# Kernel optimization log

Measured on AMD Instinct MI355X. Metric: run time of the kernel, lower is better.

## Reference

```python
import jax, jax.numpy as jnp
import numpy as np

ALPHA = 10.0
K = 10
BN_EPS = 1e-5


def _conv3d(x, w, b, pad):
    # x: [N,C,D,H,W], w: [O,I,kd,kh,kw]
    y = jax.lax.conv_general_dilated(
        x, w, window_strides=(1, 1, 1),
        padding=[(pad, pad)] * 3,
        dimension_numbers=('NCDHW', 'OIDHW', 'NCDHW'))
    return y + b[None, :, None, None, None]


def _bn(x, gamma, beta, mean, var):
    c = (None, slice(None), None, None, None)
    return gamma[c] * (x - mean[c]) * jax.lax.rsqrt(var[c] + BN_EPS) + beta[c]


def setup_inputs() -> dict:
    key = jax.random.key(0)
    ks = jax.random.split(key, 12)
    B, D, H, W = 1, 32, 32, 32
    LAT = 8
    M = 4096  # stored database vectors
    inp = {
        'bg_prob': jax.random.uniform(ks[0], (B, 1, D, H, W), jnp.float32),
        'ed_prob': jax.random.uniform(ks[1], (B, 1, D, H, W), jnp.float32),
        'context_mask': jnp.ones((B, D, H, W), dtype=bool),
        # conv1: 2 -> 16, k3
        'w1': jax.random.normal(ks[2], (16, 2, 3, 3, 3), jnp.float32) * 0.1,
        'b1': jnp.zeros((16,), jnp.float32),
        'g1': jnp.ones((16,), jnp.float32),
        'be1': jnp.zeros((16,), jnp.float32),
        'm1': jnp.zeros((16,), jnp.float32),
        'v1': jnp.ones((16,), jnp.float32),
        # conv2: 16 -> 32, k3
        'w2': jax.random.normal(ks[3], (32, 16, 3, 3, 3), jnp.float32) * 0.05,
        'b2': jnp.zeros((32,), jnp.float32),
        'g2': jnp.ones((32,), jnp.float32),
        'be2': jnp.zeros((32,), jnp.float32),
        'm2': jnp.zeros((32,), jnp.float32),
        'v2': jnp.ones((32,), jnp.float32),
        # conv3: 32 -> latent_dim, k1
        'w3': jax.random.normal(ks[4], (LAT, 32, 1, 1, 1), jnp.float32) * 0.1,
        'b3': jnp.zeros((LAT,), jnp.float32),
    }
    db = jax.random.normal(ks[5], (M, LAT), jnp.float32)
    db = db / jnp.maximum(jnp.linalg.norm(db, axis=1, keepdims=True), 1e-12)
    inp['db_feats'] = db
    inp['db_labels'] = jax.random.uniform(ks[6], (M,), jnp.float32)
    return inp


def reference(bg_prob, ed_prob, context_mask,
              w1, b1, g1, be1, m1, v1,
              w2, b2, g2, be2, m2, v2,
              w3, b3, db_feats, db_labels):
    # --- query encoder (BatchNorm in inference mode) ---
    x = jnp.concatenate([bg_prob, ed_prob], axis=1)              # [B,2,D,H,W]
    x = jax.nn.relu(_bn(_conv3d(x, w1, b1, 1), g1, be1, m1, v1))
    x = jax.nn.relu(_bn(_conv3d(x, w2, b2, 1), g2, be2, m2, v2))
    lat = _conv3d(x, w3, b3, 0)                                   # [B,C,D,H,W]
    # F.normalize(dim=1), eps=1e-12
    lat = lat / jnp.maximum(jnp.linalg.norm(lat, axis=1, keepdims=True), 1e-12)
    B, C, D, H, W = lat.shape
    q = lat.transpose(0, 2, 3, 4, 1).reshape(-1, C)               # [N,C]
    # --- exact L2 kNN (FAISS IndexFlatL2 returns squared distances) ---
    d2 = (jnp.sum(q * q, axis=1, keepdims=True)
          + jnp.sum(db_feats * db_feats, axis=1)[None, :]
          - 2.0 * q @ db_feats.T)                                 # [N,M]
    neg_top, idx = jax.lax.top_k(-d2, K)                          # k smallest
    dists = -neg_top                                              # [N,K]
    w = jnp.exp(-ALPHA * dists)
    lbl = db_labels[idx]                                          # [N,K] gather
    pred = jnp.sum(w * lbl, axis=1) / (jnp.sum(w, axis=1) + 1e-8)
    # NOTE: original view(B,2,D,H,W) is inconsistent (N=B*D*H*W preds);
    # return the consistent [B,D,H,W].
    return pred.reshape(B, D, H, W)
```

## Files before the change

kernel.cpp:

```cpp
#include <hip/hip_runtime.h>

#define ALPHA 10.0f
#define BN_EPS 1e-5f
#define NVOX 32768
#define MDB 4096
#define CAP 128

typedef __attribute__((ext_vector_type(8))) short short8;
typedef __attribute__((ext_vector_type(16))) float f32x16;

__device__ __forceinline__ unsigned short bfr(float x) {
  unsigned u = __float_as_uint(x);
  return (unsigned short)((u + 0x7FFFu + ((u >> 16) & 1u)) >> 16);
}
__device__ __forceinline__ void split3(float x, unsigned short& h,
                                       unsigned short& m, unsigned short& l) {
  h = bfr(x);
  float fh = __uint_as_float((unsigned)h << 16);
  float x1 = x - fh;
  m = bfr(x1);
  float fm = __uint_as_float((unsigned)m << 16);
  l = bfr(x1 - fm);
}

__device__ __forceinline__ f32x16 d2_tile(short8 a1, short8 a2, short8 a3,
                                          short8 a4, short8 b1, short8 b3,
                                          short8 b4) {
  f32x16 acc = {};
  acc = __builtin_amdgcn_mfma_f32_32x32x16_bf16(a4, b4, acc, 0, 0, 0);
  acc = __builtin_amdgcn_mfma_f32_32x32x16_bf16(a3, b3, acc, 0, 0, 0);
  acc = __builtin_amdgcn_mfma_f32_32x32x16_bf16(a2, b1, acc, 0, 0, 0);
  acc = __builtin_amdgcn_mfma_f32_32x32x16_bf16(a1, b1, acc, 0, 0, 0);
  return acc;
}

__device__ __forceinline__ float fmin3(float a, float b, float c) {
  return fminf(fminf(a, b), c);
}

#define INSERT2(d, va, vb)                                              \
  do {                                                                  \
    float _lo = fminf((va), (vb)), _hi = fmaxf((va), (vb));             \
    _Pragma("unroll")                                                   \
    for (int _k = 9; _k >= 2; --_k)                                     \
      d[_k] = fmin3(d[_k], fmaxf(d[_k - 1], _lo), fmaxf(d[_k - 2], _hi)); \
    d[1] = fmin3(d[1], fmaxf(d[0], _lo), _hi);                          \
    d[0] = fminf(d[0], _lo);                                            \
  } while (0)

__global__ __launch_bounds__(128) void k_conv1p(
    const float* __restrict__ bg, const float* __restrict__ ed,
    const float* __restrict__ w1, const float* __restrict__ b1,
    const float* __restrict__ g1, const float* __restrict__ be1,
    const float* __restrict__ m1, const float* __restrict__ v1,
    float* __restrict__ A, const float* __restrict__ db,
    unsigned short* __restrict__ DBH, unsigned short* __restrict__ DBM,
    unsigned short* __restrict__ DBL, unsigned short* __restrict__ DB4) {
  int t = threadIdx.x;
  if (blockIdx.x >= 256) {
    int j = (blockIdx.x - 256) * 128 + t;
    float4 x0 = ((const float4*)(db + (size_t)j * 8))[0];
    float4 x1 = ((const float4*)(db + (size_t)j * 8))[1];
    float x[8] = {x0.x, x0.y, x0.z, x0.w, x1.x, x1.y, x1.z, x1.w};
    float ss = x[0] * x[0];
#pragma unroll
    for (int i = 1; i < 8; ++i) ss = fmaf(x[i], x[i], ss);
    short8 sh = {}, sm = {}, sl = {};
#pragma unroll
    for (int i = 0; i < 8; ++i) {
      unsigned short h, m, l;
      split3(-2.f * x[i], h, m, l);
      sh[i] = (short)h; sm[i] = (short)m; sl[i] = (short)l;
    }
    unsigned short dh, dm, dl;
    split3(ss, dh, dm, dl);
    short8 s4 = {};
    s4[0] = (short)dh; s4[1] = (short)dm; s4[2] = (short)dl;
    s4[3] = (short)0x3F80; s4[4] = (short)0x3F80; s4[5] = (short)0x3F80;
    *(short8*)(DBH + (size_t)j * 8) = sh;
    *(short8*)(DBM + (size_t)j * 8) = sm;
    *(short8*)(DBL + (size_t)j * 8) = sl;
    *(short8*)(DB4 + (size_t)j * 8) = s4;
    return;
  }
  __shared__ float wT[54 * 16];
  __shared__ float sc[16], shs[16];
  for (int i = t; i < 864; i += 128) {
    int o = i & 15, r = i >> 4;
    wT[i] = w1[o * 54 + r];
  }
  if (t < 16) {
    float s = g1[t] * rsqrtf(v1[t] + BN_EPS);
    sc[t] = s;
    shs[t] = (b1[t] - m1[t]) * s + be1[t];
  }
  __syncthreads();
  int v = blockIdx.x * 128 + t;
  int x = v & 31, y = (v >> 5) & 31, z = v >> 10;
  float acc[16];
#pragma unroll
  for (int o = 0; o < 16; ++o) acc[o] = 0.f;
#pragma unroll 1
  for (int k = 0; k < 27; ++k) {
    int dz = k / 9 - 1, dy = (k / 3) % 3 - 1, dx = k % 3 - 1;
    int zz = z + dz, yy = y + dy, xx = x + dx;
    bool inb = (unsigned)zz < 32u && (unsigned)yy < 32u && (unsigned)xx < 32u;
    int vv = zz * 1024 + yy * 32 + xx;
#pragma unroll
    for (int c = 0; c < 2; ++c) {
      const float* in = c ? ed : bg;
      float val = inb ? in[vv] : 0.f;
      const float4* wp = (const float4*)&wT[(c * 27 + k) * 16];
      float4 wa = wp[0], wb = wp[1], wc = wp[2], wd = wp[3];
      acc[0] = fmaf(val, wa.x, acc[0]);  acc[1] = fmaf(val, wa.y, acc[1]);
      acc[2] = fmaf(val, wa.z, acc[2]);  acc[3] = fmaf(val, wa.w, acc[3]);
      acc[4] = fmaf(val, wb.x, acc[4]);  acc[5] = fmaf(val, wb.y, acc[5]);
      acc[6] = fmaf(val, wb.z, acc[6]);  acc[7] = fmaf(val, wb.w, acc[7]);
      acc[8] = fmaf(val, wc.x, acc[8]);  acc[9] = fmaf(val, wc.y, acc[9]);
      acc[10] = fmaf(val, wc.z, acc[10]); acc[11] = fmaf(val, wc.w, acc[11]);
      acc[12] = fmaf(val, wd.x, acc[12]); acc[13] = fmaf(val, wd.y, acc[13]);
      acc[14] = fmaf(val, wd.z, acc[14]); acc[15] = fmaf(val, wd.w, acc[15]);
    }
  }
#pragma unroll
  for (int o = 0; o < 16; ++o) {
    float y2 = fmaf(acc[o], sc[o], shs[o]);
    A[o * NVOX + v] = y2 > 0.f ? y2 : 0.f;
  }
}

__global__ __launch_bounds__(256) void k_conv2(
    const float* __restrict__ A, const float* __restrict__ w2,
    const float* __restrict__ b2, const float* __restrict__ g2,
    const float* __restrict__ be2, const float* __restrict__ m2,
    const float* __restrict__ v2, float* __restrict__ B) {
  __shared__ float wT[432 * 8];
  __shared__ float sc[8], shs[8];
  int t = threadIdx.x;
  int og = blockIdx.x >> 7;
  int vb = blockIdx.x & 127;
  for (int i = t; i < 3456; i += 256) {
    int o = i & 7, r = i >> 3;
    wT[i] = w2[(og * 8 + o) * 432 + r];
  }
  if (t < 8) {
    int o = og * 8 + t;
    float s = g2[o] * rsqrtf(v2[o] + BN_EPS);
    sc[t] = s;
    shs[t] = (b2[o] - m2[o]) * s + be2[o];
  }
  __syncthreads();
  int v = vb * 256 + t;
  int x = v & 31, y = (v >> 5) & 31, z = v >> 10;
  float acc[8];
#pragma unroll
  for (int o = 0; o < 8; ++o) acc[o] = 0.f;
#pragma unroll 1
  for (int k = 0; k < 27; ++k) {
    int dz = k / 9 - 1, dy = (k / 3) % 3 - 1, dx = k % 3 - 1;
    int zz = z + dz, yy = y + dy, xx = x + dx;
    bool inb = (unsigned)zz < 32u && (unsigned)yy < 32u && (unsigned)xx < 32u;
    int vv = zz * 1024 + yy * 32 + xx;
#pragma unroll
    for (int ci = 0; ci < 16; ++ci) {
      float val = inb ? A[ci * NVOX + vv] : 0.f;
      const float4* wp = (const float4*)&wT[(ci * 27 + k) * 8];
      float4 wa = wp[0], wb = wp[1];
      acc[0] = fmaf(val, wa.x, acc[0]); acc[1] = fmaf(val, wa.y, acc[1]);
      acc[2] = fmaf(val, wa.z, acc[2]); acc[3] = fmaf(val, wa.w, acc[3]);
      acc[4] = fmaf(val, wb.x, acc[4]); acc[5] = fmaf(val, wb.y, acc[5]);
      acc[6] = fmaf(val, wb.z, acc[6]); acc[7] = fmaf(val, wb.w, acc[7]);
    }
  }
#pragma unroll
  for (int o = 0; o < 8; ++o) {
    float y2 = fmaf(acc[o], sc[o], shs[o]);
    B[(og * 8 + o) * NVOX + v] = y2 > 0.f ? y2 : 0.f;
  }
}

__global__ __launch_bounds__(128) void k_conv3q(
    const float* __restrict__ B, const float* __restrict__ w3,
    const float* __restrict__ b3, unsigned short* __restrict__ QH,
    unsigned short* __restrict__ QM, unsigned short* __restrict__ QL,
    unsigned short* __restrict__ Q4) {
  __shared__ float wT[32 * 8];
  __shared__ float bL[8];
  int t = threadIdx.x;
  for (int i = t; i < 256; i += 128) {
    int o = i & 7, ci = i >> 3;
    wT[i] = w3[o * 32 + ci];
  }
  if (t < 8) bL[t] = b3[t];
  __syncthreads();
  int v = blockIdx.x * 128 + t;
  float lat[8];
#pragma unroll
  for (int o = 0; o < 8; ++o) lat[o] = bL[o];
#pragma unroll 4
  for (int ci = 0; ci < 32; ++ci) {
    float val = B[ci * NVOX + v];
    const float4* wp = (const float4*)&wT[ci * 8];
    float4 wa = wp[0], wb = wp[1];
    lat[0] = fmaf(val, wa.x, lat[0]); lat[1] = fmaf(val, wa.y, lat[1]);
    lat[2] = fmaf(val, wa.z, lat[2]); lat[3] = fmaf(val, wa.w, lat[3]);
    lat[4] = fmaf(val, wb.x, lat[4]); lat[5] = fmaf(val, wb.y, lat[5]);
    lat[6] = fmaf(val, wb.z, lat[6]); lat[7] = fmaf(val, wb.w, lat[7]);
  }
  float n2 = 0.f;
#pragma unroll
  for (int o = 0; o < 8; ++o) n2 = fmaf(lat[o], lat[o], n2);
  float inv = 1.f / fmaxf(sqrtf(n2), 1e-12f);
  float q[8];
#pragma unroll
  for (int o = 0; o < 8; ++o) q[o] = lat[o] * inv;
  float qq = q[0] * q[0];
#pragma unroll
  for (int o = 1; o < 8; ++o) qq = fmaf(q[o], q[o], qq);
  short8 sh = {}, sm = {}, sl = {};
#pragma unroll
  for (int o = 0; o < 8; ++o) {
    unsigned short h, m, l;
    split3(q[o], h, m, l);
    sh[o] = (short)h; sm[o] = (short)m; sl[o] = (short)l;
  }
  unsigned short qh, qm, ql;
  split3(qq, qh, qm, ql);
  short8 s4 = {};
  s4[0] = (short)0x3F80; s4[1] = (short)0x3F80; s4[2] = (short)0x3F80;
  s4[3] = (short)qh; s4[4] = (short)qm; s4[5] = (short)ql;
  *(short8*)(QH + (size_t)v * 8) = sh;
  *(short8*)(QM + (size_t)v * 8) = sm;
  *(short8*)(QL + (size_t)v * 8) = sl;
  *(short8*)(Q4 + (size_t)v * 8) = s4;
}

__global__ __launch_bounds__(512) void k_knn_fused(
    const unsigned short* __restrict__ QH, const unsigned short* __restrict__ QM,
    const unsigned short* __restrict__ QL, const unsigned short* __restrict__ Q4,
    const unsigned short* __restrict__ DBH, const unsigned short* __restrict__ DBM,
    const unsigned short* __restrict__ DBL, const unsigned short* __restrict__ DB4,
    const float* __restrict__ labels, float* __restrict__ out) {
  __shared__ float smem[2 * 32 * (CAP + 1)];
  __shared__ float T0L[32];
  __shared__ int cnt[32];
  float (*listd)[CAP + 1] = (float (*)[CAP + 1])smem;
  int (*listi)[CAP + 1] = (int (*)[CAP + 1])(smem + 32 * (CAP + 1));
  float (*lds_top)[10][32] = (float (*)[10][32])smem;
  int t = threadIdx.x, w = t >> 6, l = t & 63;
  int lo32 = l & 31, hi = l >> 5;
  int q = blockIdx.x * 32 + lo32;
  if (t < 32) cnt[t] = 0;
  short8 zz = {};
  short8 b1 = *(const short8*)((hi ? QM : QH) + (size_t)q * 8);
  short8 b3 = *(const short8*)((hi ? QL : QH) + (size_t)q * 8);
  short8 b4v = *(const short8*)(Q4 + (size_t)q * 8);
  short8 b4 = hi ? zz : b4v;
  int r0 = w * 512;

  float d[10];
#pragma unroll
  for (int k = 0; k < 10; ++k) d[k] = 3.4e38f;
#pragma unroll 1
  for (int tt = 0; tt < 4; ++tt) {
    int r = r0 + tt * 32 + lo32;
    short8 a1 = *(const short8*)(DBH + (size_t)r * 8);
    short8 a2 = *(const short8*)(DBM + (size_t)r * 8);
    short8 a3 = *(const short8*)((hi ? DBH : DBL) + (size_t)r * 8);
    short8 a4 = *(const short8*)(DB4 + (size_t)r * 8);
    f32x16 acc = d2_tile(a1, a2, a3, a4, b1, b3, b4);
#pragma unroll
    for (int p = 0; p < 8; ++p) INSERT2(d, acc[2 * p], acc[2 * p + 1]);
  }
  {
    float e[10];
#pragma unroll
    for (int k = 0; k < 10; ++k) e[k] = __shfl_xor(d[k], 32);
#pragma unroll
    for (int k = 0; k < 10; k += 2) INSERT2(d, e[k], e[k + 1]);
  }
  if (l < 32) {
#pragma unroll
    for (int k = 0; k < 10; ++k) lds_top[w][k][lo32] = d[k];
  }
  __syncthreads();
  if (t < 32) {
    float m[10];
#pragma unroll
    for (int k = 0; k < 10; ++k) m[k] = 3.4e38f;
#pragma unroll 1
    for (int w2 = 0; w2 < 8; ++w2) {
#pragma unroll
      for (int k2 = 0; k2 < 10; k2 += 2)
        INSERT2(m, lds_top[w2][k2][t], lds_top[w2][k2 + 1][t]);
    }
    T0L[t] = m[9];
  }
  __syncthreads();
  float T0q = T0L[lo32];

#pragma unroll 1
  for (int tt = 0; tt < 16; ++tt) {
    int r = r0 + tt * 32 + lo32;
    short8 a1 = *(const short8*)(DBH + (size_t)r * 8);
    short8 a2 = *(const short8*)(DBM + (size_t)r * 8);
    short8 a3 = *(const short8*)((hi ? DBH : DBL) + (size_t)r * 8);
    short8 a4 = *(const short8*)(DB4 + (size_t)r * 8);
    f32x16 acc = d2_tile(a1, a2, a3, a4, b1, b3, b4);
    int rb = r0 + tt * 32 + 4 * hi;
#pragma unroll
    for (int i = 0; i < 16; ++i) {
      float d2v = acc[i];
      bool p = d2v <= T0q;
      if (__any(p)) {
        if (p) {
          int slot = atomicAdd(&cnt[lo32], 1);
          if (slot < CAP) {
            listd[lo32][slot] = d2v;
            listi[lo32][slot] = rb + (i & 3) + 8 * (i >> 2);
          }
        }
      }
    }
  }
  __syncthreads();

  {
    int qc = t >> 4, s0 = t & 15;
    int n = min(cnt[qc], CAP);
    for (int s = s0; s < n; s += 16) {
      int idx = listi[qc][s];
      ((float*)listi[qc])[s] = labels[idx];
    }
  }
  __syncthreads();

  if (t < 32) {
    int n = min(cnt[t], CAP);
    float dd[10];
#pragma unroll
    for (int k = 0; k < 10; ++k) dd[k] = 3.4e38f;
    int j = 0;
#pragma unroll 1
    for (; j + 1 < n; j += 2) INSERT2(dd, listd[t][j], listd[t][j + 1]);
    if (j < n) INSERT2(dd, listd[t][j], 3.4e38f);
    float Tv = dd[9];
    const float C2 = -14.4269504088896340736f;
    float num = 0.f, den = 0.f;
#pragma unroll 1
    for (int j2 = 0; j2 < n; ++j2) {
      float v = listd[t][j2];
      if (v <= Tv) {
        float e = exp2f(v * C2);
        den += e;
        num = fmaf(e, ((float*)listi[t])[j2], num);
      }
    }
    out[blockIdx.x * 32 + t] = num / (den + 1e-8f);
  }
}

extern "C" void kernel_launch(void* const* d_in, const int* in_sizes, int n_in,
                              void* d_out, int out_size, void* d_ws, size_t ws_size,
                              hipStream_t stream) {
  const float* bg = (const float*)d_in[0];
  const float* ed = (const float*)d_in[1];
  const float* w1 = (const float*)d_in[3];
  const float* b1 = (const float*)d_in[4];
  const float* g1 = (const float*)d_in[5];
  const float* be1 = (const float*)d_in[6];
  const float* m1 = (const float*)d_in[7];
  const float* v1 = (const float*)d_in[8];
  const float* w2 = (const float*)d_in[9];
  const float* b2 = (const float*)d_in[10];
  const float* g2 = (const float*)d_in[11];
  const float* be2 = (const float*)d_in[12];
  const float* m2 = (const float*)d_in[13];
  const float* v2 = (const float*)d_in[14];
  const float* w3 = (const float*)d_in[15];
  const float* b3 = (const float*)d_in[16];
  const float* db = (const float*)d_in[17];
  const float* labels = (const float*)d_in[18];
  float* out = (float*)d_out;

  char* ws = (char*)d_ws;
  const size_t MB = 1024 * 1024;
  float* A = (float*)(ws + 0);
  float* B = (float*)(ws + 2 * MB);
  unsigned short* QH = (unsigned short*)(ws + 0);
  unsigned short* QM = QH + (size_t)NVOX * 8;
  unsigned short* QL = QM + (size_t)NVOX * 8;
  unsigned short* Q4 = QL + (size_t)NVOX * 8;
  unsigned short* DBH = (unsigned short*)(ws + 6 * MB);
  unsigned short* DBM = DBH + (size_t)MDB * 8;
  unsigned short* DBL = DBM + (size_t)MDB * 8;
  unsigned short* DB4 = DBL + (size_t)MDB * 8;

  k_conv1p<<<288, 128, 0, stream>>>(bg, ed, w1, b1, g1, be1, m1, v1, A, db,
                                    DBH, DBM, DBL, DB4);
  k_conv2<<<4 * 128, 256, 0, stream>>>(A, w2, b2, g2, be2, m2, v2, B);
  k_conv3q<<<256, 128, 0, stream>>>(B, w3, b3, QH, QM, QL, Q4);
  k_knn_fused<<<NVOX / 32, 512, 0, stream>>>(QH, QM, QL, Q4, DBH, DBM, DBL,
                                             DB4, labels, out);
}
```

Before: 115.7 us.

## Fuse 1x1 conv and query normalization into kNN kernel, parallelize label weighting

The separate conv3q kernel is removed. Each kNN block now computes the 1x1 conv, L2 normalization and bf16 three-way split for its 32 queries in shared memory, which saves a launch and the round trip of query data through global memory. The final weighted sum is split across 16 threads per query with a partial-sum reduction, instead of one thread doing a serial label gather. Conv1 moves to 256-thread blocks, and the warp-uniform __any check around candidate insertion is dropped. The cost is extra syncs and shared-memory work inside the kNN kernel, and smem aliasing that has to stay correct.

```diff
diff --git a/kernel.cpp b/kernel.cpp
--- a/kernel.cpp
+++ b/kernel.cpp
@@ -48,7 +48,7 @@
     d[0] = fminf(d[0], _lo);                                            \
   } while (0)
 
-__global__ __launch_bounds__(128) void k_conv1p(
+__global__ __launch_bounds__(256) void k_conv1p(
     const float* __restrict__ bg, const float* __restrict__ ed,
     const float* __restrict__ w1, const float* __restrict__ b1,
     const float* __restrict__ g1, const float* __restrict__ be1,
@@ -57,8 +57,8 @@
     unsigned short* __restrict__ DBH, unsigned short* __restrict__ DBM,
     unsigned short* __restrict__ DBL, unsigned short* __restrict__ DB4) {
   int t = threadIdx.x;
-  if (blockIdx.x >= 256) {
-    int j = (blockIdx.x - 256) * 128 + t;
+  if (blockIdx.x >= 128) {
+    int j = (blockIdx.x - 128) * 256 + t;
     float4 x0 = ((const float4*)(db + (size_t)j * 8))[0];
     float4 x1 = ((const float4*)(db + (size_t)j * 8))[1];
     float x[8] = {x0.x, x0.y, x0.z, x0.w, x1.x, x1.y, x1.z, x1.w};
@@ -85,7 +85,7 @@
   }
   __shared__ float wT[54 * 16];
   __shared__ float sc[16], shs[16];
-  for (int i = t; i < 864; i += 128) {
+  for (int i = t; i < 864; i += 256) {
     int o = i & 15, r = i >> 4;
     wT[i] = w1[o * 54 + r];
   }
@@ -95,7 +95,7 @@
     shs[t] = (b1[t] - m1[t]) * s + be1[t];
   }
   __syncthreads();
-  int v = blockIdx.x * 128 + t;
+  int v = blockIdx.x * 256 + t;
   int x = v & 31, y = (v >> 5) & 31, z = v >> 10;
   float acc[16];
 #pragma unroll
@@ -179,83 +179,86 @@
   }
 }
 
-__global__ __launch_bounds__(128) void k_conv3q(
+__global__ __launch_bounds__(512) void k_knn_fused(
     const float* __restrict__ B, const float* __restrict__ w3,
-    const float* __restrict__ b3, unsigned short* __restrict__ QH,
-    unsigned short* __restrict__ QM, unsigned short* __restrict__ QL,
-    unsigned short* __restrict__ Q4) {
-  __shared__ float wT[32 * 8];
-  __shared__ float bL[8];
-  int t = threadIdx.x;
-  for (int i = t; i < 256; i += 128) {
-    int o = i & 7, ci = i >> 3;
-    wT[i] = w3[o * 32 + ci];
-  }
-  if (t < 8) bL[t] = b3[t];
-  __syncthreads();
-  int v = blockIdx.x * 128 + t;
-  float lat[8];
-#pragma unroll
-  for (int o = 0; o < 8; ++o) lat[o] = bL[o];
-#pragma unroll 4
-  for (int ci = 0; ci < 32; ++ci) {
-    float val = B[ci * NVOX + v];
-    const float4* wp = (const float4*)&wT[ci * 8];
-    float4 wa = wp[0], wb = wp[1];
-    lat[0] = fmaf(val, wa.x, lat[0]); lat[1] = fmaf(val, wa.y, lat[1]);
-    lat[2] = fmaf(val, wa.z, lat[2]); lat[3] = fmaf(val, wa.w, lat[3]);
-    lat[4] = fmaf(val, wb.x, lat[4]); lat[5] = fmaf(val, wb.y, lat[5]);
-    lat[6] = fmaf(val, wb.z, lat[6]); lat[7] = fmaf(val, wb.w, lat[7]);
-  }
-  float n2 = 0.f;
-#pragma unroll
-  for (int o = 0; o < 8; ++o) n2 = fmaf(lat[o], lat[o], n2);
-  float inv = 1.f / fmaxf(sqrtf(n2), 1e-12f);
-  float q[8];
-#pragma unroll
-  for (int o = 0; o < 8; ++o) q[o] = lat[o] * inv;
-  float qq = q[0] * q[0];
-#pragma unroll
-  for (int o = 1; o < 8; ++o) qq = fmaf(q[o], q[o], qq);
-  short8 sh = {}, sm = {}, sl = {};
-#pragma unroll
-  for (int o = 0; o < 8; ++o) {
-    unsigned short h, m, l;
-    split3(q[o], h, m, l);
-    sh[o] = (short)h; sm[o] = (short)m; sl[o] = (short)l;
-  }
-  unsigned short qh, qm, ql;
-  split3(qq, qh, qm, ql);
-  short8 s4 = {};
-  s4[0] = (short)0x3F80; s4[1] = (short)0x3F80; s4[2] = (short)0x3F80;
-  s4[3] = (short)qh; s4[4] = (short)qm; s4[5] = (short)ql;
-  *(short8*)(QH + (size_t)v * 8) = sh;
-  *(short8*)(QM + (size_t)v * 8) = sm;
-  *(short8*)(QL + (size_t)v * 8) = sl;
-  *(short8*)(Q4 + (size_t)v * 8) = s4;
-}
-
-__global__ __launch_bounds__(512) void k_knn_fused(
-    const unsigned short* __restrict__ QH, const unsigned short* __restrict__ QM,
-    const unsigned short* __restrict__ QL, const unsigned short* __restrict__ Q4,
+    const float* __restrict__ b3c,
     const unsigned short* __restrict__ DBH, const unsigned short* __restrict__ DBM,
     const unsigned short* __restrict__ DBL, const unsigned short* __restrict__ DB4,
     const float* __restrict__ labels, float* __restrict__ out) {
   __shared__ float smem[2 * 32 * (CAP + 1)];
   __shared__ float T0L[32];
   __shared__ int cnt[32];
+  __shared__ float pn[32][16];
   float (*listd)[CAP + 1] = (float (*)[CAP + 1])smem;
   int (*listi)[CAP + 1] = (int (*)[CAP + 1])(smem + 32 * (CAP + 1));
   float (*lds_top)[10][32] = (float (*)[10][32])smem;
+  float* pt = smem;
+  float* latL = smem + 4096;
+  float* wTl = smem + 4352;
+  float* bLl = smem + 4608;
+  unsigned short* qf = (unsigned short*)(smem + 4616);
+
   int t = threadIdx.x, w = t >> 6, l = t & 63;
   int lo32 = l & 31, hi = l >> 5;
-  int q = blockIdx.x * 32 + lo32;
   if (t < 32) cnt[t] = 0;
+
+  if (t < 256) wTl[(t >> 3) * 8 + (t & 7)] = w3[(t & 7) * 32 + (t >> 3)];
+  if (t < 8) bLl[t] = b3c[t];
+  __syncthreads();
+  {
+    int qq_ = t & 31, g = t >> 5;
+    int v = blockIdx.x * 32 + qq_;
+    float v0 = B[(size_t)(2 * g) * NVOX + v];
+    float v1 = B[(size_t)(2 * g + 1) * NVOX + v];
+    const float* w0 = &wTl[(2 * g) * 8];
+    const float* w1p = &wTl[(2 * g + 1) * 8];
+#pragma unroll
+    for (int o = 0; o < 8; ++o)
+      pt[(qq_ * 8 + o) * 16 + g] = fmaf(v1, w1p[o], v0 * w0[o]);
+  }
+  __syncthreads();
+  if (t < 256) {
+    int qq_ = t >> 3, o = t & 7;
+    float s = bLl[o];
+#pragma unroll
+    for (int g = 0; g < 16; ++g) s += pt[(qq_ * 8 + o) * 16 + g];
+    latL[qq_ * 8 + o] = s;
+  }
+  __syncthreads();
+  if (t < 32) {
+    float lat[8];
+#pragma unroll
+    for (int o = 0; o < 8; ++o) lat[o] = latL[t * 8 + o];
+    float n2 = 0.f;
+#pragma unroll
+    for (int o = 0; o < 8; ++o) n2 = fmaf(lat[o], lat[o], n2);
+    float inv = 1.f / fmaxf(sqrtf(n2), 1e-12f);
+    float qv[8];
+#pragma unroll
+    for (int o = 0; o < 8; ++o) qv[o] = lat[o] * inv;
+    float qq2 = qv[0] * qv[0];
+#pragma unroll
+    for (int o = 1; o < 8; ++o) qq2 = fmaf(qv[o], qv[o], qq2);
+    unsigned short h, m, lo;
+#pragma unroll
+    for (int o = 0; o < 8; ++o) {
+      split3(qv[o], h, m, lo);
+      qf[(t * 4 + 0) * 8 + o] = h;
+      qf[(t * 4 + 1) * 8 + o] = m;
+      qf[(t * 4 + 2) * 8 + o] = lo;
+    }
+    split3(qq2, h, m, lo);
+    qf[(t * 4 + 3) * 8 + 0] = 0x3F80; qf[(t * 4 + 3) * 8 + 1] = 0x3F80;
+    qf[(t * 4 + 3) * 8 + 2] = 0x3F80; qf[(t * 4 + 3) * 8 + 3] = h;
+    qf[(t * 4 + 3) * 8 + 4] = m;      qf[(t * 4 + 3) * 8 + 5] = lo;
+    qf[(t * 4 + 3) * 8 + 6] = 0;      qf[(t * 4 + 3) * 8 + 7] = 0;
+  }
+  __syncthreads();
   short8 zz = {};
-  short8 b1 = *(const short8*)((hi ? QM : QH) + (size_t)q * 8);
-  short8 b3 = *(const short8*)((hi ? QL : QH) + (size_t)q * 8);
-  short8 b4v = *(const short8*)(Q4 + (size_t)q * 8);
-  short8 b4 = hi ? zz : b4v;
+  short8 b1 = *(const short8*)&qf[((size_t)lo32 * 4 + (hi ? 1 : 0)) * 8];
+  short8 b3 = *(const short8*)&qf[((size_t)lo32 * 4 + (hi ? 2 : 0)) * 8];
+  short8 b4 = hi ? zz : *(const short8*)&qf[((size_t)lo32 * 4 + 3) * 8];
+  __syncthreads();
   int r0 = w * 512;
 
   float d[10];
@@ -311,30 +314,18 @@
 #pragma unroll
     for (int i = 0; i < 16; ++i) {
       float d2v = acc[i];
-      bool p = d2v <= T0q;
-      if (__any(p)) {
-        if (p) {
-          int slot = atomicAdd(&cnt[lo32], 1);
-          if (slot < CAP) {
-            listd[lo32][slot] = d2v;
-            listi[lo32][slot] = rb + (i & 3) + 8 * (i >> 2);
-          }
+      if (d2v <= T0q) {
+        int slot = atomicAdd(&cnt[lo32], 1);
+        if (slot < CAP) {
+          listd[lo32][slot] = d2v;
+          listi[lo32][slot] = rb + (i & 3) + 8 * (i >> 2);
         }
       }
     }
   }
   __syncthreads();
 
-  {
-    int qc = t >> 4, s0 = t & 15;
-    int n = min(cnt[qc], CAP);
-    for (int s = s0; s < n; s += 16) {
-      int idx = listi[qc][s];
-      ((float*)listi[qc])[s] = labels[idx];
-    }
-  }
-  __syncthreads();
-
+  float Tv = 0.f, den = 0.f;
   if (t < 32) {
     int n = min(cnt[t], CAP);
     float dd[10];
@@ -344,18 +335,31 @@
 #pragma unroll 1
     for (; j + 1 < n; j += 2) INSERT2(dd, listd[t][j], listd[t][j + 1]);
     if (j < n) INSERT2(dd, listd[t][j], 3.4e38f);
-    float Tv = dd[9];
+    Tv = dd[9];
     const float C2 = -14.4269504088896340736f;
-    float num = 0.f, den = 0.f;
-#pragma unroll 1
-    for (int j2 = 0; j2 < n; ++j2) {
-      float v = listd[t][j2];
-      if (v <= Tv) {
-        float e = exp2f(v * C2);
-        den += e;
-        num = fmaf(e, ((float*)listi[t])[j2], num);
-      }
-    }
+#pragma unroll
+    for (int k = 0; k < 10; ++k) den += exp2f(dd[k] * C2);
+    T0L[t] = Tv;
+  }
+  __syncthreads();
+
+  {
+    const float C2 = -14.4269504088896340736f;
+    int qc = t >> 4, s0 = t & 15;
+    int n = min(cnt[qc], CAP);
+    float Tq = T0L[qc];
+    float nump = 0.f;
+    for (int s = s0; s < n; s += 16) {
+      float v = listd[qc][s];
+      if (v <= Tq) nump = fmaf(exp2f(v * C2), labels[listi[qc][s]], nump);
+    }
+    pn[qc][s0] = nump;
+  }
+  __syncthreads();
+  if (t < 32) {
+    float num = 0.f;
+#pragma unroll
+    for (int g = 0; g < 16; ++g) num += pn[t][g];
     out[blockIdx.x * 32 + t] = num / (den + 1e-8f);
   }
 }
@@ -387,19 +391,14 @@
   const size_t MB = 1024 * 1024;
   float* A = (float*)(ws + 0);
   float* B = (float*)(ws + 2 * MB);
-  unsigned short* QH = (unsigned short*)(ws + 0);
-  unsigned short* QM = QH + (size_t)NVOX * 8;
-  unsigned short* QL = QM + (size_t)NVOX * 8;
-  unsigned short* Q4 = QL + (size_t)NVOX * 8;
   unsigned short* DBH = (unsigned short*)(ws + 6 * MB);
   unsigned short* DBM = DBH + (size_t)MDB * 8;
   unsigned short* DBL = DBM + (size_t)MDB * 8;
   unsigned short* DB4 = DBL + (size_t)MDB * 8;
 
-  k_conv1p<<<288, 128, 0, stream>>>(bg, ed, w1, b1, g1, be1, m1, v1, A, db,
+  k_conv1p<<<144, 256, 0, stream>>>(bg, ed, w1, b1, g1, be1, m1, v1, A, db,
                                     DBH, DBM, DBL, DB4);
   k_conv2<<<4 * 128, 256, 0, stream>>>(A, w2, b2, g2, be2, m2, v2, B);
-  k_conv3q<<<256, 128, 0, stream>>>(B, w3, b3, QH, QM, QL, Q4);
-  k_knn_fused<<<NVOX / 32, 512, 0, stream>>>(QH, QM, QL, Q4, DBH, DBM, DBL,
-                                             DB4, labels, out);
-}
+  k_knn_fused<<<NVOX / 32, 512, 0, stream>>>(B, w3, b3, DBH, DBM, DBL, DB4,
+                                             labels, out);
+}
```

New measurement: 118.4 us. +2.3%, slower.
